# Performance work log

Hardware: AMD Instinct MI355X
Metric: run time of the kernel (lower is better)

The kernel has to match this reference:

```python
import jax, jax.numpy as jnp
import numpy as np

TARGET_SPARSITY = 0.9
LN_EPS = 1e-5


def ternary_quant(W):
    """BitNet-b1.58 style ternary quantization: W -> {-1,0,+1} * mean(|W|).
    Straight-through estimator so gradients pass to the latent weights."""
    scale = jnp.mean(jnp.abs(W))
    q = jnp.clip(jnp.round(W / (scale + 1e-8)), -1.0, 1.0) * scale
    return W + jax.lax.stop_gradient(q - W)


def layernorm(x, gamma, beta):
    mu = jnp.mean(x, axis=-1, keepdims=True)
    var = jnp.var(x, axis=-1, keepdims=True)
    return (x - mu) * jax.lax.rsqrt(var + LN_EPS) * gamma + beta


def setup_inputs() -> dict:
    key = jax.random.key(0)
    ks = jax.random.split(key, 3)
    B, S, D, N = 4, 2048, 2048, 8192
    x = jax.random.normal(ks[0], (B, S, D), dtype=jnp.float32)
    W_syn = jax.random.normal(ks[1], (N, D), dtype=jnp.float32) * (1.0 / np.sqrt(D))
    b_syn = jnp.zeros((N,), dtype=jnp.float32)
    W_out = jax.random.normal(ks[2], (D, N), dtype=jnp.float32) * (1.0 / np.sqrt(N))
    b_out = jnp.zeros((D,), dtype=jnp.float32)
    gamma = jnp.ones((D,), dtype=jnp.float32)
    beta = jnp.zeros((D,), dtype=jnp.float32)
    return {"x": x, "W_syn": W_syn, "b_syn": b_syn, "W_out": W_out,
            "b_out": b_out, "gamma": gamma, "beta": beta}


def reference(x, W_syn, b_syn, W_out, b_out, gamma, beta):
    B, S, D = x.shape
    N = W_syn.shape[0]
    x_flat = x.reshape(-1, D)  # [T, D], T = B*S

    # RNU: ternary-weight synapses + sparse firing (keep top (1-sparsity) per token)
    z = x_flat @ ternary_quant(W_syn).T + b_syn  # [T, N]
    k = max(1, int(N * (1.0 - TARGET_SPARSITY)))
    topv, _ = jax.lax.top_k(z, k)                 # [T, k]
    thresh = topv[:, -1:]                          # k-th largest per token
    hidden = jnp.where(z >= thresh, jax.nn.relu(z), 0.0)  # sparse firing rates

    # Ternary output projection
    out = hidden @ ternary_quant(W_out).T + b_out  # [T, D]
    out = out.reshape(B, S, D)

    # Residual + LayerNorm
    return layernorm(x + out, gamma, beta)
```

## Files before the change

### kernel.cpp

```cpp
#include <hip/hip_runtime.h>


typedef __attribute__((ext_vector_type(8))) short short8;
typedef __attribute__((ext_vector_type(4))) float f32x4;

__device__ __forceinline__ float bf2f(unsigned h) {
    return __uint_as_float(h << 16);
}
__device__ __forceinline__ unsigned f2bf(float f) {
    unsigned u = __float_as_uint(f);
    return (u + 0x7fffu + ((u >> 16) & 1u)) >> 16;
}

typedef __attribute__((address_space(1))) const void gq_void;
typedef __attribute__((address_space(3))) void ls_void;
__device__ __forceinline__ void gload16(const void* g, void* l) {
    __builtin_amdgcn_global_load_lds((gq_void*)g, (ls_void*)l, 16, 0, 0);
}

__global__ __launch_bounds__(64) void init_detect(float* sc, const unsigned* g_raw,
                                                  int* flag) {
    if (threadIdx.x < 16) sc[threadIdx.x] = 0.0f;
    if (threadIdx.x == 0) *flag = (g_raw[0] == 0x3F803F80u) ? 1 : 0;
}

__global__ __launch_bounds__(256) void split_x(const void* __restrict__ src,
                                               unsigned short* __restrict__ hi,
                                               unsigned short* __restrict__ lo, int n,
                                               const int* __restrict__ flagp) {
    const int flag = *flagp;
    int idx = blockIdx.x * 256 + threadIdx.x;
    int stride = gridDim.x * 256;
    if (flag) {
        const uint4* s = (const uint4*)src;
        uint4* dh = (uint4*)hi;
        uint4* dl = (uint4*)lo;
        uint4 zz; zz.x = zz.y = zz.z = zz.w = 0u;
        for (int i = idx; i < n / 8; i += stride) { dh[i] = s[i]; dl[i] = zz; }
    } else {
        const float4* s = (const float4*)src;
        uint2* dh = (uint2*)hi;
        uint2* dl = (uint2*)lo;
        for (int i = idx; i < n / 4; i += stride) {
            float4 v = s[i];
            unsigned h0 = f2bf(v.x), h1 = f2bf(v.y), h2 = f2bf(v.z), h3 = f2bf(v.w);
            unsigned l0 = f2bf(v.x - bf2f(h0));
            unsigned l1 = f2bf(v.y - bf2f(h1));
            unsigned l2 = f2bf(v.z - bf2f(h2));
            unsigned l3 = f2bf(v.w - bf2f(h3));
            uint2 oh; oh.x = h0 | (h1 << 16); oh.y = h2 | (h3 << 16);
            uint2 ol; ol.x = l0 | (l1 << 16); ol.y = l2 | (l3 << 16);
            dh[i] = oh;
            dl[i] = ol;
        }
    }
}

__global__ __launch_bounds__(256) void to_f32_all(
    const void* __restrict__ b1, float* __restrict__ d1, int n1,
    const void* __restrict__ b2, float* __restrict__ d2, int n2,
    const void* __restrict__ b3, float* __restrict__ d3, int n3,
    const void* __restrict__ b4, float* __restrict__ d4, int n4,
    const int* __restrict__ flagp) {
    const int flag = *flagp;
    int i = blockIdx.x * 256 + threadIdx.x;
    if (flag) {
        if (i < n1) d1[i] = bf2f((unsigned)((const unsigned short*)b1)[i]);
        if (i < n2) d2[i] = bf2f((unsigned)((const unsigned short*)b2)[i]);
        if (i < n3) d3[i] = bf2f((unsigned)((const unsigned short*)b3)[i]);
        if (i < n4) d4[i] = bf2f((unsigned)((const unsigned short*)b4)[i]);
    } else {
        if (i < n1) d1[i] = ((const float*)b1)[i];
        if (i < n2) d2[i] = ((const float*)b2)[i];
        if (i < n3) d3[i] = ((const float*)b3)[i];
        if (i < n4) d4[i] = ((const float*)b4)[i];
    }
}

__global__ __launch_bounds__(256) void abs_sum_any(const void* __restrict__ w, int n,
                                                   float* __restrict__ out,
                                                   const int* __restrict__ flagp) {
    const int flag = *flagp;
    int idx = blockIdx.x * 256 + threadIdx.x;
    int stride = gridDim.x * 256;
    float s = 0.0f;
    if (flag) {
        const uint4* wv = (const uint4*)w;
        for (int c = idx; c < n / 8; c += stride) {
            uint4 v = wv[c];
            unsigned a[4] = {v.x, v.y, v.z, v.w};
#pragma unroll
            for (int j = 0; j < 4; j++)
                s += fabsf(bf2f(a[j] & 0xffffu)) + fabsf(bf2f(a[j] >> 16));
        }
    } else {
        const float4* wv = (const float4*)w;
        for (int c = idx; c < n / 4; c += stride) {
            float4 v = wv[c];
            s += fabsf(v.x) + fabsf(v.y) + fabsf(v.z) + fabsf(v.w);
        }
    }
#pragma unroll
    for (int off = 32; off; off >>= 1) s += __shfl_down(s, off);
    __shared__ float red[4];
    int lane = threadIdx.x & 63, wv_id = threadIdx.x >> 6;
    if (lane == 0) red[wv_id] = s;
    __syncthreads();
    if (threadIdx.x == 0) atomicAdd(out, red[0] + red[1] + red[2] + red[3]);
}

__global__ __launch_bounds__(64) void finalize_scale(float* sc, float inv_count) {
    if (threadIdx.x == 0) {
        sc[2] = sc[0] * inv_count;
        sc[3] = sc[1] * inv_count;
    }
}

__global__ __launch_bounds__(256) void quantize_any(const void* __restrict__ w,
                                                    unsigned short* __restrict__ q,
                                                    const float* __restrict__ sc, int idx,
                                                    int n, const int* __restrict__ flagp) {
    const int flag = *flagp;
    const float d = sc[idx] + 1e-8f;
    int i = blockIdx.x * 256 + threadIdx.x;
    int stride = gridDim.x * 256;
    if (flag) {
        const uint4* wv = (const uint4*)w;
        uint4* qv = (uint4*)q;
        for (; i < n / 8; i += stride) {
            uint4 v = wv[i];
            unsigned a[4] = {v.x, v.y, v.z, v.w};
            unsigned r[4];
#pragma unroll
            for (int j = 0; j < 4; j++) {
                float lo = bf2f(a[j] & 0xffffu);
                float hi = bf2f(a[j] >> 16);
                float rl = fminf(1.0f, fmaxf(-1.0f, rintf(lo / d)));
                float rh = fminf(1.0f, fmaxf(-1.0f, rintf(hi / d)));
                r[j] = f2bf(rl) | (f2bf(rh) << 16);
            }
            uint4 o;
            o.x = r[0]; o.y = r[1]; o.z = r[2]; o.w = r[3];
            qv[i] = o;
        }
    } else {
        const float4* wv = (const float4*)w;
        uint2* qv = (uint2*)q;
        for (; i < n / 4; i += stride) {
            float4 v = wv[i];
            float r0 = fminf(1.0f, fmaxf(-1.0f, rintf(v.x / d)));
            float r1 = fminf(1.0f, fmaxf(-1.0f, rintf(v.y / d)));
            float r2 = fminf(1.0f, fmaxf(-1.0f, rintf(v.z / d)));
            float r3 = fminf(1.0f, fmaxf(-1.0f, rintf(v.w / d)));
            uint2 o;
            o.x = f2bf(r0) | (f2bf(r1) << 16);
            o.y = f2bf(r2) | (f2bf(r3) << 16);
            qv[i] = o;
        }
    }
}

template <int BM, int BN, bool TWO, int KSPLIT>
__global__ __launch_bounds__(256) void gemm_bt_t(const unsigned short* __restrict__ A0,
                                                 const unsigned short* __restrict__ A1,
                                                 const unsigned short* __restrict__ B,
                                                 float* __restrict__ C, size_t cstride,
                                                 const float* __restrict__ biasf,
                                                 const float* __restrict__ scp, int scidx,
                                                 int N, int K) {
    constexpr int WM = BM / 2;
    constexpr int WN = BN / 2;
    constexpr int AM = WM / 16;
    constexpr int AN = WN / 16;
    __shared__ uint4 sA[BM * 8];
    __shared__ uint4 sL[TWO ? BM * 8 : 4];
    __shared__ uint4 sB[BN * 8];
    const int tid = threadIdx.x;
    const int lane = tid & 63;
    const int wave = tid >> 6;
    const int wm = (wave >> 1) * WM;
    const int wn = (wave & 1) * WN;
    const int l15 = lane & 15;
    const int quad = lane >> 4;

    int bx = blockIdx.x, by = blockIdx.y;
    {
        const int gx = gridDim.x, gy = gridDim.y;
        if ((gx & 7) == 0) {
            int orig = by * gx + bx;
            int cpx = gx >> 3;
            int xcd = orig & 7;
            int pos = orig >> 3;
            bx = xcd * cpx + pos / gy;
            by = pos % gy;
        }
    }
    const int m0 = by * BM;
    const int n0 = bx * BN;

    const int kz = (KSPLIT > 1) ? (int)blockIdx.z : 0;
    const int kper = K / KSPLIT;
    const int kbeg = kz * kper;
    const int kend = kbeg + kper;
    float* __restrict__ Cw = C + (size_t)kz * cstride;

    f32x4 acc[AM][AN];
#pragma unroll
    for (int i = 0; i < AM; i++)
#pragma unroll
        for (int j = 0; j < AN; j++) acc[i][j] = (f32x4){0.f, 0.f, 0.f, 0.f};

    const unsigned short* Abase = A0 + (size_t)m0 * K;
    const unsigned short* Lbase = TWO ? (A1 + (size_t)m0 * K) : nullptr;
    const unsigned short* Bbase = B + (size_t)n0 * K;

    for (int k0 = kbeg; k0 < kend; k0 += 64) {
#pragma unroll
        for (int i = 0; i < BM * 8 / 256; i++) {
            int s = tid + i * 256;
            int r = s >> 3, c = s & 7;
            size_t go = (size_t)r * K + k0 + c * 8;
            gload16(Abase + go, sA + i * 256 + wave * 64);
            if (TWO) gload16(Lbase + go, sL + i * 256 + wave * 64);
        }
#pragma unroll
        for (int i = 0; i < BN * 8 / 256; i++) {
            int s = tid + i * 256;
            int r = s >> 3, c = s & 7;
            size_t go = (size_t)r * K + k0 + c * 8;
            gload16(Bbase + go, sB + i * 256 + wave * 64);
        }
        __syncthreads();
#pragma unroll
        for (int kk = 0; kk < 64; kk += 32) {
            const int jj = (kk >> 3) + quad;
            short8 ah[AM], bfr[AN];
#pragma unroll
            for (int t = 0; t < AM; t++)
                ah[t] = *(const short8*)&sA[(wm + t * 16 + l15) * 8 + jj];
#pragma unroll
            for (int t = 0; t < AN; t++)
                bfr[t] = *(const short8*)&sB[(wn + t * 16 + l15) * 8 + jj];
#pragma unroll
            for (int im = 0; im < AM; im++)
#pragma unroll
                for (int in = 0; in < AN; in++)
                    acc[im][in] = __builtin_amdgcn_mfma_f32_16x16x32_bf16(
                        ah[im], bfr[in], acc[im][in], 0, 0, 0);
            if (TWO) {
                short8 al[AM];
#pragma unroll
                for (int t = 0; t < AM; t++)
                    al[t] = *(const short8*)&sL[(wm + t * 16 + l15) * 8 + jj];
#pragma unroll
                for (int im = 0; im < AM; im++)
#pragma unroll
                    for (int in = 0; in < AN; in++)
                        acc[im][in] = __builtin_amdgcn_mfma_f32_16x16x32_bf16(
                            al[im], bfr[in], acc[im][in], 0, 0, 0);
            }
        }
        __syncthreads();
    }

    float scale = scp[scidx];
#pragma unroll
    for (int in = 0; in < AN; in++) {
        int col = n0 + wn + in * 16 + l15;
        float bv = (kz == 0) ? biasf[col] : 0.0f;
#pragma unroll
        for (int im = 0; im < AM; im++) {
            int rbase = m0 + wm + im * 16 + quad * 4;
#pragma unroll
            for (int r = 0; r < 4; r++) {
                Cw[(size_t)(rbase + r) * N + col] = scale * acc[im][in][r] + bv;
            }
        }
    }
}

__global__ __launch_bounds__(256) void topk_hidden(const float* __restrict__ z,
                                                   unsigned short* __restrict__ hidden,
                                                   int N, int k) {
    __shared__ unsigned keys[8192];
    __shared__ unsigned hist[2048];
    __shared__ unsigned wsum[4];
    __shared__ unsigned cand[256];
    __shared__ unsigned sh_want, sh_kk, sh_cnt, sh_nc, sh_kth;
    const int tid = threadIdx.x;
    const int lane = tid & 63;
    const int wv = tid >> 6;
    const size_t row = blockIdx.x;
    const float* zr = z + row * (size_t)N;

    auto select_bucket = [&](int nbins, int shift) {
        const int cs = nbins >> 8;
        const int base = tid * cs;
        unsigned cv = 0;
        for (int j = 0; j < cs; j++) cv += hist[base + j];
        unsigned v = cv;
#pragma unroll
        for (int off = 1; off < 64; off <<= 1) {
            unsigned o = __shfl_down(v, off);
            if (lane + off < 64) v += o;
        }
        unsigned kk = sh_kk;
        if (lane == 0) wsum[wv] = v;
        __syncthreads();
        unsigned higher = 0;
        for (int w = wv + 1; w < 4; w++) higher += wsum[w];
        unsigned incl = v + higher;
        unsigned excl = incl - cv;
        if (excl < kk && kk <= incl) {
            unsigned running = excl;
            for (int b = base + cs - 1; b >= base; b--) {
                unsigned h = hist[b];
                if (running + h >= kk) {
                    sh_want = sh_want | ((unsigned)b << shift);
                    sh_kk = kk - running;
                    sh_cnt = h;
                    break;
                }
                running += h;
            }
        }
        __syncthreads();
    };

    for (int b = tid; b < 2048; b += 256) hist[b] = 0u;
    if (tid == 0) { sh_want = 0u; sh_kk = (unsigned)k; }
    __syncthreads();
    const float4* zv = (const float4*)zr;
    for (int i = tid; i < N / 4; i += 256) {
        float4 f = zv[i];
        unsigned u0 = __float_as_uint(f.x); u0 = (u0 & 0x80000000u) ? ~u0 : (u0 | 0x80000000u);
        unsigned u1 = __float_as_uint(f.y); u1 = (u1 & 0x80000000u) ? ~u1 : (u1 | 0x80000000u);
        unsigned u2 = __float_as_uint(f.z); u2 = (u2 & 0x80000000u) ? ~u2 : (u2 | 0x80000000u);
        unsigned u3 = __float_as_uint(f.w); u3 = (u3 & 0x80000000u) ? ~u3 : (u3 | 0x80000000u);
        keys[i * 4 + 0] = u0; keys[i * 4 + 1] = u1;
        keys[i * 4 + 2] = u2; keys[i * 4 + 3] = u3;
        atomicAdd(&hist[u0 >> 21], 1u);
        atomicAdd(&hist[u1 >> 21], 1u);
        atomicAdd(&hist[u2 >> 21], 1u);
        atomicAdd(&hist[u3 >> 21], 1u);
    }
    __syncthreads();
    select_bucket(2048, 21);

    for (int b = tid; b < 2048; b += 256) hist[b] = 0u;
    __syncthreads();
    {
        const unsigned want0 = sh_want;
        for (int i = tid; i < N; i += 256) {
            unsigned u = keys[i];
            if ((u >> 21) == (want0 >> 21)) atomicAdd(&hist[(u >> 10) & 2047u], 1u);
        }
    }
    __syncthreads();
    select_bucket(2048, 10);

    const unsigned want = sh_want;
    const unsigned cnt = sh_cnt;
    if (tid == 0) sh_nc = 0u;
    __syncthreads();
    if (cnt <= 256u) {
        for (int i = tid; i < N; i += 256) {
            unsigned u = keys[i];
            if ((u >> 10) == (want >> 10)) {
                unsigned p = atomicAdd(&sh_nc, 1u);
                if (p < 256u) cand[p] = u;
            }
        }
        __syncthreads();
        const unsigned kk = sh_kk;
        const int nc = (int)sh_nc;
        if (tid < nc) {
            unsigned vvv = cand[tid];
            unsigned g = 0, ge = 0;
            for (int j = 0; j < nc; j++) {
                g += (cand[j] > vvv) ? 1u : 0u;
                ge += (cand[j] >= vvv) ? 1u : 0u;
            }
            if (g < kk && kk <= ge) sh_kth = vvv;
        }
        __syncthreads();
    } else {
        for (int b = tid; b < 1024; b += 256) hist[b] = 0u;
        __syncthreads();
        for (int i = tid; i < N; i += 256) {
            unsigned u = keys[i];
            if ((u >> 10) == (want >> 10)) atomicAdd(&hist[u & 1023u], 1u);
        }
        __syncthreads();
        select_bucket(1024, 0);
        if (tid == 0) sh_kth = sh_want;
        __syncthreads();
    }
    const unsigned kth = sh_kth;

    unsigned short* hr = hidden + row * (size_t)N;
    uint2* hr2 = (uint2*)hr;
    for (int i = tid; i < N / 4; i += 256) {
        unsigned u0 = keys[i * 4 + 0], u1 = keys[i * 4 + 1];
        unsigned u2 = keys[i * 4 + 2], u3 = keys[i * 4 + 3];
        float f0 = (u0 & 0x80000000u) ? __uint_as_float(u0 & 0x7fffffffu) : __uint_as_float(~u0);
        float f1 = (u1 & 0x80000000u) ? __uint_as_float(u1 & 0x7fffffffu) : __uint_as_float(~u1);
        float f2 = (u2 & 0x80000000u) ? __uint_as_float(u2 & 0x7fffffffu) : __uint_as_float(~u2);
        float f3 = (u3 & 0x80000000u) ? __uint_as_float(u3 & 0x7fffffffu) : __uint_as_float(~u3);
        float h0 = (u0 >= kth) ? fmaxf(f0, 0.0f) : 0.0f;
        float h1 = (u1 >= kth) ? fmaxf(f1, 0.0f) : 0.0f;
        float h2 = (u2 >= kth) ? fmaxf(f2, 0.0f) : 0.0f;
        float h3 = (u3 >= kth) ? fmaxf(f3, 0.0f) : 0.0f;
        uint2 o;
        o.x = f2bf(h0) | (f2bf(h1) << 16);
        o.y = f2bf(h2) | (f2bf(h3) << 16);
        hr2[i] = o;
    }
}

__global__ __launch_bounds__(256) void ln_kernel(const unsigned short* __restrict__ xh,
                                                 const unsigned short* __restrict__ xl,
                                                 const float* __restrict__ o,
                                                 size_t cstride,
                                                 const float* __restrict__ gamma,
                                                 const float* __restrict__ beta,
                                                 float* __restrict__ y, int D) {
    const int tid = threadIdx.x;
    const size_t row = blockIdx.x;
    const unsigned short* xhr = xh + row * (size_t)D;
    const unsigned short* xlr = xl + row * (size_t)D;
    const float* orow = o + row * (size_t)D;
    float v[8];
    float s = 0.0f, s2 = 0.0f;
#pragma unroll
    for (int j = 0; j < 8; j++) {
        int i = tid + j * 256;
        float val = bf2f((unsigned)xhr[i]) + bf2f((unsigned)xlr[i]);
        val += orow[i] + orow[i + cstride] + orow[i + 2 * cstride] + orow[i + 3 * cstride];
        v[j] = val;
        s += val;
        s2 += val * val;
    }
#pragma unroll
    for (int off = 32; off; off >>= 1) {
        s += __shfl_down(s, off);
        s2 += __shfl_down(s2, off);
    }
    __shared__ float red[8];
    int lane = tid & 63, wv = tid >> 6;
    if (lane == 0) { red[wv] = s; red[4 + wv] = s2; }
    __syncthreads();
    float S = red[0] + red[1] + red[2] + red[3];
    float S2 = red[4] + red[5] + red[6] + red[7];
    float mu = S / (float)D;
    float var = S2 / (float)D - mu * mu;
    float inv = rsqrtf(var + 1e-5f);
#pragma unroll
    for (int j = 0; j < 8; j++) {
        int i = tid + j * 256;
        y[row * (size_t)D + i] = (v[j] - mu) * inv * gamma[i] + beta[i];
    }
}

extern "C" void kernel_launch(void* const* d_in, const int* in_sizes, int n_in,
                              void* d_out, int out_size, void* d_ws, size_t ws_size,
                              hipStream_t stream) {
    const void* x_raw = d_in[0];
    const void* Wsyn_raw = d_in[1];
    const void* bsyn_raw = d_in[2];
    const void* Wout_raw = d_in[3];
    const void* bout_raw = d_in[4];
    const void* gamma_raw = d_in[5];
    const void* beta_raw = d_in[6];
    float* out = (float*)d_out;

    const int M = 8192, D = 2048, N = 8192, K1 = 2048;
    const int kTop = 819;
    const int NW = M * D;

    char* wsb = (char*)d_ws;
    float* sc = (float*)wsb;
    int* flag = (int*)(wsb + 128);
    float* gamma_f = (float*)(wsb + 4096);
    float* beta_f = (float*)(wsb + 12288);
    float* bout_f = (float*)(wsb + 20480);
    float* bsyn_f = (float*)(wsb + 28672);
    unsigned short* x_hi = (unsigned short*)(wsb + 65536);
    unsigned short* x_lo = (unsigned short*)(wsb + 65536 + 1ull * 33554432ull);
    unsigned short* qsyn = (unsigned short*)(wsb + 65536 + 2ull * 33554432ull);
    unsigned short* qout = (unsigned short*)(wsb + 65536 + 3ull * 33554432ull);
    const size_t FIXED = 65536 + 4ull * 33554432ull;

    const size_t per_row = (size_t)N * 4 + (size_t)N * 2;
    size_t avail = (ws_size > FIXED) ? ws_size - FIXED : 0;
    long mc = (long)(avail / per_row);
    mc &= ~127L;
    if (mc > M) mc = M;
    if (mc < 128) mc = 128;
    const int Mc = (int)mc;
    char* chunk_base = wsb + FIXED;

    init_detect<<<1, 64, 0, stream>>>(sc, (const unsigned*)gamma_raw, flag);

    split_x<<<2048, 256, 0, stream>>>(x_raw, x_hi, x_lo, M * D, flag);
    to_f32_all<<<(N + 255) / 256, 256, 0, stream>>>(bsyn_raw, bsyn_f, N, bout_raw,
                                                    bout_f, D, gamma_raw, gamma_f, D,
                                                    beta_raw, beta_f, D, flag);

    abs_sum_any<<<2048, 256, 0, stream>>>(Wsyn_raw, NW, sc + 0, flag);
    abs_sum_any<<<2048, 256, 0, stream>>>(Wout_raw, NW, sc + 1, flag);
    finalize_scale<<<1, 64, 0, stream>>>(sc, 1.0f / 16777216.0f);
    quantize_any<<<2048, 256, 0, stream>>>(Wsyn_raw, qsyn, sc, 2, NW, flag);
    quantize_any<<<2048, 256, 0, stream>>>(Wout_raw, qout, sc, 3, NW, flag);

    for (int m0 = 0; m0 < M; m0 += Mc) {
        const int rows = (M - m0 < Mc) ? (M - m0) : Mc;
        float* z = (float*)chunk_base;
        unsigned short* hidden = (unsigned short*)(chunk_base + (size_t)Mc * N * 4);
        float* outf = (float*)chunk_base;
        const size_t cstride = (size_t)rows * D;

        dim3 g1(N / 128, rows / 128);
        gemm_bt_t<128, 128, true, 1><<<g1, 256, 0, stream>>>(
            x_hi + (size_t)m0 * K1, x_lo + (size_t)m0 * K1, qsyn, z, 0, bsyn_f,
            sc, 2, N, K1);

        topk_hidden<<<rows, 256, 0, stream>>>(z, hidden, N, kTop);

        dim3 g2(D / 128, rows / 128, 4);
        gemm_bt_t<128, 128, false, 4><<<g2, 256, 0, stream>>>(
            hidden, nullptr, qout, outf, cstride, bout_f, sc, 3, D, N);

        ln_kernel<<<rows, 256, 0, stream>>>(x_hi + (size_t)m0 * D, x_lo + (size_t)m0 * D,
                                            outf, cstride, gamma_f, beta_f,
                                            out + (size_t)m0 * D, D);
    }
}
```

Baseline: 1.799 ms.

## Remove XCD block remap in GEMM and use warp-aggregated histogram atomics

```diff
diff --git a/kernel.cpp b/kernel.cpp
--- a/kernel.cpp
+++ b/kernel.cpp
@@ -180,23 +180,10 @@
     const int wave = tid >> 6;
     const int wm = (wave >> 1) * WM;
     const int wn = (wave & 1) * WN;
+    const int m0 = blockIdx.y * BM;
+    const int n0 = blockIdx.x * BN;
     const int l15 = lane & 15;
     const int quad = lane >> 4;
-
-    int bx = blockIdx.x, by = blockIdx.y;
-    {
-        const int gx = gridDim.x, gy = gridDim.y;
-        if ((gx & 7) == 0) {
-            int orig = by * gx + bx;
-            int cpx = gx >> 3;
-            int xcd = orig & 7;
-            int pos = orig >> 3;
-            bx = xcd * cpx + pos / gy;
-            by = pos % gy;
-        }
-    }
-    const int m0 = by * BM;
-    const int n0 = bx * BN;
 
     const int kz = (KSPLIT > 1) ? (int)blockIdx.z : 0;
     const int kper = K / KSPLIT;
@@ -292,6 +279,17 @@
     const int wv = tid >> 6;
     const size_t row = blockIdx.x;
     const float* zr = z + row * (size_t)N;
+
+    auto aggAdd = [&](unsigned bin) {
+        unsigned long long todo = __ballot(1);
+        while (todo) {
+            int leader = __ffsll((long long)todo) - 1;
+            unsigned lb = __shfl(bin, leader);
+            unsigned long long eq = __ballot(bin == lb);
+            if (lane == leader) atomicAdd(&hist[lb], (unsigned)__popcll(eq));
+            todo &= ~eq;
+        }
+    };
 
     auto select_bucket = [&](int nbins, int shift) {
         const int cs = nbins >> 8;
@@ -339,10 +337,10 @@
         unsigned u3 = __float_as_uint(f.w); u3 = (u3 & 0x80000000u) ? ~u3 : (u3 | 0x80000000u);
         keys[i * 4 + 0] = u0; keys[i * 4 + 1] = u1;
         keys[i * 4 + 2] = u2; keys[i * 4 + 3] = u3;
-        atomicAdd(&hist[u0 >> 21], 1u);
-        atomicAdd(&hist[u1 >> 21], 1u);
-        atomicAdd(&hist[u2 >> 21], 1u);
-        atomicAdd(&hist[u3 >> 21], 1u);
+        aggAdd(u0 >> 21);
+        aggAdd(u1 >> 21);
+        aggAdd(u2 >> 21);
+        aggAdd(u3 >> 21);
     }
     __syncthreads();
     select_bucket(2048, 21);
```

After: 2.858 ms. 58.9% more time.
